# Kernel tuning notes

Measured on AMD Instinct MI355X. Metric: run time of the kernel, lower is better.

Reference implementation:

```python
import jax, jax.numpy as jnp
import numpy as np

N_HEADS = 16
EMB_DIM = 2048
HEAD_DIM = EMB_DIM // N_HEADS  # 128
SEQ_LEN = 2048


def _init_tensor(key, size, scale_dim=0):
    # matches torch: (2*rand - 1) / sqrt(size[scale_dim])
    u = jax.random.uniform(key, size, dtype=jnp.float32)
    return (2.0 * u - 1.0) / jnp.sqrt(jnp.float32(size[scale_dim]))


def setup_inputs() -> dict:
    key = jax.random.key(0)
    kx, kq, kk, kv, ko = jax.random.split(key, 5)
    X = jax.random.normal(kx, (1, SEQ_LEN, EMB_DIM), dtype=jnp.float32)
    W_Q = _init_tensor(kq, (N_HEADS, EMB_DIM, HEAD_DIM), scale_dim=1)
    W_K = _init_tensor(kk, (N_HEADS, EMB_DIM, HEAD_DIM), scale_dim=1)
    W_V = _init_tensor(kv, (N_HEADS, EMB_DIM, HEAD_DIM), scale_dim=1)
    W_out = _init_tensor(ko, (EMB_DIM, EMB_DIM), scale_dim=0)
    return {"X": X, "W_Q": W_Q, "W_K": W_K, "W_V": W_V, "W_out": W_out}


def reference(X, W_Q, W_K, W_V, W_out):
    # X: (1, t, d); W_Q/K/V: (n, d, h); broadcast matmul -> (n, t, h)
    x = X[0]  # (t, d)
    Q = jnp.einsum('td,ndh->nth', x, W_Q)
    K = jnp.einsum('td,ndh->nth', x, W_K)
    V = jnp.einsum('td,ndh->nth', x, W_V)
    scale = 1.0 / jnp.sqrt(jnp.float32(HEAD_DIM))
    Z = jnp.einsum('nth,nsh->nts', Q, K) * scale  # (n, t, t)
    A = jax.nn.softmax(Z, axis=-1)
    R = jnp.einsum('nts,nsh->nth', A, V)  # (n, t, h)
    t = R.shape[1]
    X_cat = jnp.transpose(R, (1, 0, 2)).reshape(t, N_HEADS * HEAD_DIM)  # (t, d)
    return X_cat @ W_out  # (t, d)
```

## Files before the change

### kernel.cpp

```cpp
#include <hip/hip_runtime.h>


typedef unsigned short u16;
typedef __bf16 bf16x8 __attribute__((ext_vector_type(8)));
typedef float f32x4 __attribute__((ext_vector_type(4)));
typedef __attribute__((address_space(1))) void gvoid;
typedef __attribute__((address_space(3))) void svoid;

union B8 { uint4 u; uint2 d[2]; bf16x8 b; };

__device__ __forceinline__ u16 f2b(float f) {
  unsigned int u = __float_as_uint(f);
  unsigned int r = (u + 0x7FFFu + ((u >> 16) & 1u)) >> 16;
  return (u16)r;
}

__global__ __launch_bounds__(256) void prep_kernel(const float* __restrict__ X,
                                                   const float* __restrict__ WQ,
                                                   const float* __restrict__ WK,
                                                   const float* __restrict__ WV,
                                                   const float* __restrict__ WO,
                                                   u16* __restrict__ Xb,
                                                   u16* __restrict__ Wqkvb,
                                                   u16* __restrict__ Woutb) {
  int bid = blockIdx.x;
  int seg = bid >> 12;
  int sub = bid & 4095;
  int tid = threadIdx.x;
  if (seg == 0) {
    int i = (sub * 256 + tid) * 4;
    float4 v = *(const float4*)(X + i);
    ushort4 o;
    o.x = f2b(v.x); o.y = f2b(v.y); o.z = f2b(v.z); o.w = f2b(v.w);
    *(ushort4*)(Xb + i) = o;
    return;
  }
  __shared__ float t[32][33];
  const float* S;
  u16* D;
  int N, n0, k0;
  if (seg <= 3) {
    const float* W = (seg == 1) ? WQ : (seg == 2) ? WK : WV;
    int head = sub >> 8, rest = sub & 255;
    N = 128;
    S = W + (size_t)head * 2048 * 128;
    D = Wqkvb + (size_t)(seg - 1) * 16 * 2048 * 128 + (size_t)head * 2048 * 128;
    n0 = (rest & 3) * 32;
    k0 = (rest >> 2) * 32;
  } else {
    N = 2048;
    S = WO;
    D = Woutb;
    n0 = (sub & 63) * 32;
    k0 = (sub >> 6) * 32;
  }
  int tx = tid & 31, ty = tid >> 5;
#pragma unroll
  for (int d = 0; d < 4; ++d)
    t[ty + d * 8][tx] = S[(size_t)(k0 + ty + d * 8) * N + n0 + tx];
  __syncthreads();
#pragma unroll
  for (int d = 0; d < 4; ++d)
    D[(size_t)(n0 + ty + d * 8) * 2048 + k0 + tx] = f2b(t[tx][ty + d * 8]);
}

__device__ __forceinline__ void stage_tile(const u16* Ag, const u16* Bg,
                                           u16* As, u16* Bs, int k0, int tid) {
#pragma unroll
  for (int it = 0; it < 4; ++it) {
    int s = it * 256 + tid;
    int pb = s * 16;
    int lb = pb ^ ((((pb) >> 7) & 7) << 4);
    int row = lb >> 7;
    int k8 = (lb >> 4) & 7;
    const u16* ga = Ag + (size_t)row * 2048 + k0 + k8 * 8;
    const u16* gb = Bg + (size_t)row * 2048 + k0 + k8 * 8;
    char* la = (char*)As + it * 4096 + (tid & 192) * 16;
    char* lb2 = (char*)Bs + it * 4096 + (tid & 192) * 16;
    __builtin_amdgcn_global_load_lds((gvoid*)(void*)ga, (svoid*)la, 16, 0, 0);
    __builtin_amdgcn_global_load_lds((gvoid*)(void*)gb, (svoid*)lb2, 16, 0, 0);
  }
}

__device__ __forceinline__ void compute_tile(const u16* As, const u16* Bs,
                                             f32x4 acc[4][4], int lane, int wr, int wc) {
#pragma unroll
  for (int ks = 0; ks < 2; ++ks) {
    B8 a[4], b[4];
#pragma unroll
    for (int i = 0; i < 4; ++i) {
      int rowa = wr * 64 + i * 16 + (lane & 15);
      int ba = rowa * 128 + ks * 64 + (lane >> 4) * 16;
      ba ^= (rowa & 7) << 4;
      a[i].u = *(const uint4*)((const char*)As + ba);
      int rowb = wc * 64 + i * 16 + (lane & 15);
      int bb = rowb * 128 + ks * 64 + (lane >> 4) * 16;
      bb ^= (rowb & 7) << 4;
      b[i].u = *(const uint4*)((const char*)Bs + bb);
    }
    __builtin_amdgcn_s_setprio(1);
#pragma unroll
    for (int i = 0; i < 4; ++i)
#pragma unroll
      for (int j = 0; j < 4; ++j)
        acc[i][j] = __builtin_amdgcn_mfma_f32_16x16x32_bf16(a[i].b, b[j].b, acc[i][j], 0, 0, 0);
    __builtin_amdgcn_s_setprio(0);
  }
}

__device__ __forceinline__ void gemm_mainloop(const u16* Ag, const u16* Bg,
                                              u16* As, u16* Bs,
                                              f32x4 acc[4][4], int tid) {
  const int lane = tid & 63;
  const int wr = tid >> 7, wc = (tid >> 6) & 1;
  for (int k0 = 0; k0 < 2048; k0 += 64) {
    __syncthreads();
    stage_tile(Ag, Bg, As, Bs, k0, tid);
    __syncthreads();
    compute_tile(As, Bs, acc, lane, wr, wc);
  }
}

__device__ __forceinline__ void gemm_mainloop_dbuf(const u16* Ag, const u16* Bg,
                                                   u16* As0, u16* Bs0, u16* As1, u16* Bs1,
                                                   f32x4 acc[4][4], int tid) {
  const int lane = tid & 63;
  const int wr = tid >> 7, wc = (tid >> 6) & 1;
  stage_tile(Ag, Bg, As0, Bs0, 0, tid);
  __syncthreads();
  for (int i = 0; i < 32; ++i) {
    u16* Ac = (i & 1) ? As1 : As0;
    u16* Bc = (i & 1) ? Bs1 : Bs0;
    u16* An = (i & 1) ? As0 : As1;
    u16* Bn = (i & 1) ? Bs0 : Bs1;
    if (i < 31) stage_tile(Ag, Bg, An, Bn, (i + 1) * 64, tid);
    compute_tile(Ac, Bc, acc, lane, wr, wc);
    __syncthreads();
  }
}

__global__ __launch_bounds__(256) void qkv_gemm_kernel(const u16* __restrict__ Xb,
                                                       const u16* __restrict__ Wb,
                                                       u16* __restrict__ Qb,
                                                       u16* __restrict__ Kb,
                                                       u16* __restrict__ VTb) {
  __shared__ __align__(16) u16 As[128 * 64];
  __shared__ __align__(16) u16 Bs[128 * 64];
  int tid = threadIdx.x;
  int o = blockIdx.x;
  int swz = (o & 7) * 96 + (o >> 3);
  int m0 = (swz & 15) * 128;
  int c0 = swz >> 4;
  int tau = c0 >> 4, head = c0 & 15;
  f32x4 z = {0.f, 0.f, 0.f, 0.f};
  f32x4 acc[4][4];
#pragma unroll
  for (int i = 0; i < 4; ++i)
#pragma unroll
    for (int j = 0; j < 4; ++j) acc[i][j] = z;
  gemm_mainloop(Xb + (size_t)m0 * 2048, Wb + (size_t)c0 * 128 * 2048, As, Bs, acc, tid);

  int lane = tid & 63, wr = tid >> 7, wc = (tid >> 6) & 1;
  if (tau < 2) {
    u16* Oh = ((tau == 0) ? Qb : Kb) + (size_t)head * 2048 * 128;
    float sc = (tau == 0) ? 0.08838834764831845f : 1.0f;
#pragma unroll
    for (int i = 0; i < 4; ++i) {
      int rb = m0 + wr * 64 + i * 16 + (lane >> 4) * 4;
#pragma unroll
      for (int j = 0; j < 4; ++j) {
        int col = wc * 64 + j * 16 + (lane & 15);
#pragma unroll
        for (int r = 0; r < 4; ++r)
          Oh[(size_t)(rb + r) * 128 + col] = f2b(acc[i][j][r] * sc);
      }
    }
  } else {
    u16* Vh = VTb + (size_t)head * 128 * 2048;
#pragma unroll
    for (int i = 0; i < 4; ++i) {
      int rb = m0 + wr * 64 + i * 16 + (lane >> 4) * 4;
#pragma unroll
      for (int j = 0; j < 4; ++j) {
        int col = wc * 64 + j * 16 + (lane & 15);
        ushort4 v;
        v.x = f2b(acc[i][j][0]); v.y = f2b(acc[i][j][1]);
        v.z = f2b(acc[i][j][2]); v.w = f2b(acc[i][j][3]);
        *(ushort4*)(Vh + (size_t)col * 2048 + rb) = v;
      }
    }
  }
}

__global__ __launch_bounds__(256, 2) void attn_kernel(const u16* __restrict__ Qb,
                                                      const u16* __restrict__ Kb,
                                                      const u16* __restrict__ VTb,
                                                      u16* __restrict__ Rb) {
  __shared__ __align__(16) u16 Ks[2][64 * 128];
  __shared__ __align__(16) u16 Vs[2][128 * 64];
  __shared__ __align__(16) u16 Ps[4 * 16 * 68];
  int tid = threadIdx.x, lane = tid & 63, w = tid >> 6;
  int bid = blockIdx.x;
  int swz = (bid & 7) * 64 + (bid >> 3);
  int head = swz >> 5;
  int q0 = (swz & 31) * 64;
  const u16* Qh = Qb + (size_t)head * 2048 * 128;
  const u16* Kh = Kb + (size_t)head * 2048 * 128;
  const u16* Vh = VTb + (size_t)head * 128 * 2048;

  B8 q[4];
  {
    int qrow = q0 + w * 16 + (lane & 15);
#pragma unroll
    for (int ks = 0; ks < 4; ++ks)
      q[ks].u = *(const uint4*)(Qh + (size_t)qrow * 128 + ks * 32 + (lane >> 4) * 8);
  }

  f32x4 o[8];
  f32x4 z4 = {0.f, 0.f, 0.f, 0.f};
#pragma unroll
  for (int f = 0; f < 8; ++f) o[f] = z4;
  float m_run[4] = {-1e30f, -1e30f, -1e30f, -1e30f};
  float l_run[4] = {0.f, 0.f, 0.f, 0.f};

  auto STAGE = [&](int bi, int s0) {
#pragma unroll
    for (int it2 = 0; it2 < 4; ++it2) {
      int pb = (it2 * 256 + tid) * 16;
      int lbK = pb ^ (((pb >> 8) & 7) << 4);
      int rowK = lbK >> 8;
      int k8 = (lbK >> 4) & 15;
      const u16* gk = Kh + (size_t)(s0 + rowK) * 128 + k8 * 8;
      char* dk = (char*)Ks[bi] + it2 * 4096 + (tid & 192) * 16;
      __builtin_amdgcn_global_load_lds((gvoid*)(void*)gk, (svoid*)dk, 16, 0, 0);
      int lbV = pb ^ (((pb >> 7) & 7) << 4);
      int rowV = lbV >> 7;
      int t8 = (lbV >> 4) & 7;
      const u16* gv = Vh + (size_t)rowV * 2048 + s0 + t8 * 8;
      char* dv = (char*)Vs[bi] + it2 * 4096 + (tid & 192) * 16;
      __builtin_amdgcn_global_load_lds((gvoid*)(void*)gv, (svoid*)dv, 16, 0, 0);
    }
  };

  STAGE(0, 0);
  __syncthreads();

  u16* Pw = Ps + w * 16 * 68;
  for (int it = 0; it < 32; ++it) {
    int cur = it & 1;
    if (it < 31) STAGE(cur ^ 1, (it + 1) * 64);

    f32x4 s[4];
#pragma unroll
    for (int f = 0; f < 4; ++f) s[f] = z4;
    __builtin_amdgcn_s_setprio(1);
#pragma unroll
    for (int f = 0; f < 4; ++f) {
      int r = f * 16 + (lane & 15);
#pragma unroll
      for (int ks = 0; ks < 4; ++ks) {
        int lb = r * 256 + ks * 64 + (lane >> 4) * 16;
        B8 kb;
        kb.u = *(const uint4*)((const char*)Ks[cur] + (lb ^ ((r & 7) << 4)));
        s[f] = __builtin_amdgcn_mfma_f32_16x16x32_bf16(q[ks].b, kb.b, s[f], 0, 0, 0);
      }
    }
    __builtin_amdgcn_s_setprio(0);

    float mt[4];
#pragma unroll
    for (int i = 0; i < 4; ++i)
      mt[i] = fmaxf(fmaxf(s[0][i], s[1][i]), fmaxf(s[2][i], s[3][i]));
#pragma unroll
    for (int mask = 1; mask <= 8; mask <<= 1)
#pragma unroll
      for (int i = 0; i < 4; ++i) mt[i] = fmaxf(mt[i], __shfl_xor(mt[i], mask, 64));

    float al[4];
#pragma unroll
    for (int i = 0; i < 4; ++i) {
      float mn = fmaxf(m_run[i], mt[i]);
      al[i] = __expf(m_run[i] - mn);
      m_run[i] = mn;
    }
    float ps[4] = {0.f, 0.f, 0.f, 0.f};
#pragma unroll
    for (int f = 0; f < 4; ++f)
#pragma unroll
      for (int i = 0; i < 4; ++i) {
        float p = __expf(s[f][i] - m_run[i]);
        ps[i] += p;
        Pw[((lane >> 4) * 4 + i) * 68 + f * 16 + (lane & 15)] = f2b(p);
      }
#pragma unroll
    for (int mask = 1; mask <= 8; mask <<= 1)
#pragma unroll
      for (int i = 0; i < 4; ++i) ps[i] += __shfl_xor(ps[i], mask, 64);
#pragma unroll
    for (int i = 0; i < 4; ++i) l_run[i] = l_run[i] * al[i] + ps[i];

#pragma unroll
    for (int f = 0; f < 8; ++f)
#pragma unroll
      for (int i = 0; i < 4; ++i) o[f][i] *= al[i];

    B8 pa[2];
#pragma unroll
    for (int k2 = 0; k2 < 2; ++k2) {
      const u16* pp = Pw + (lane & 15) * 68 + k2 * 32 + (lane >> 4) * 8;
      pa[k2].d[0] = *(const uint2*)(pp);
      pa[k2].d[1] = *(const uint2*)(pp + 4);
    }
    __builtin_amdgcn_s_setprio(1);
#pragma unroll
    for (int f = 0; f < 8; ++f) {
      int r = f * 16 + (lane & 15);
#pragma unroll
      for (int k2 = 0; k2 < 2; ++k2) {
        int lb = r * 128 + k2 * 64 + (lane >> 4) * 16;
        B8 vb;
        vb.u = *(const uint4*)((const char*)Vs[cur] + (lb ^ ((r & 7) << 4)));
        o[f] = __builtin_amdgcn_mfma_f32_16x16x32_bf16(pa[k2].b, vb.b, o[f], 0, 0, 0);
      }
    }
    __builtin_amdgcn_s_setprio(0);

    __syncthreads();
  }

#pragma unroll
  for (int i = 0; i < 4; ++i) {
    float inv = 1.0f / l_run[i];
    int row = q0 + w * 16 + (lane >> 4) * 4 + i;
#pragma unroll
    for (int f = 0; f < 8; ++f) {
      int col = head * 128 + f * 16 + (lane & 15);
      Rb[(size_t)row * 2048 + col] = f2b(o[f][i] * inv);
    }
  }
}

__global__ __launch_bounds__(256) void out_gemm_kernel(const u16* __restrict__ Rb,
                                                       const u16* __restrict__ Wob,
                                                       float* __restrict__ out) {
  __shared__ __align__(16) u16 As[2][128 * 64];
  __shared__ __align__(16) u16 Bs[2][128 * 64];
  int tid = threadIdx.x;
  int o = blockIdx.x;
  int swz = (o & 7) * 32 + (o >> 3);
  int m0 = (swz & 15) * 128, n0 = (swz >> 4) * 128;
  f32x4 z = {0.f, 0.f, 0.f, 0.f};
  f32x4 acc[4][4];
#pragma unroll
  for (int i = 0; i < 4; ++i)
#pragma unroll
    for (int j = 0; j < 4; ++j) acc[i][j] = z;
  gemm_mainloop_dbuf(Rb + (size_t)m0 * 2048, Wob + (size_t)n0 * 2048,
                     As[0], Bs[0], As[1], Bs[1], acc, tid);

  int lane = tid & 63, wr = tid >> 7, wc = (tid >> 6) & 1;
#pragma unroll
  for (int i = 0; i < 4; ++i) {
    int rb = m0 + wr * 64 + i * 16 + (lane >> 4) * 4;
#pragma unroll
    for (int j = 0; j < 4; ++j) {
      int col = n0 + wc * 64 + j * 16 + (lane & 15);
#pragma unroll
      for (int r = 0; r < 4; ++r)
        out[(size_t)(rb + r) * 2048 + col] = acc[i][j][r];
    }
  }
}

extern "C" void kernel_launch(void* const* d_in, const int* in_sizes, int n_in,
                              void* d_out, int out_size, void* d_ws, size_t ws_size,
                              hipStream_t stream) {
  const float* X  = (const float*)d_in[0];
  const float* WQ = (const float*)d_in[1];
  const float* WK = (const float*)d_in[2];
  const float* WV = (const float*)d_in[3];
  const float* WO = (const float*)d_in[4];
  float* out = (float*)d_out;

  char* ws = (char*)d_ws;
  const size_t MB8 = 8u << 20;
  u16* Xb    = (u16*)(ws);
  u16* Wqkvb = (u16*)(ws + MB8);
  u16* Woutb = (u16*)(ws + 4 * MB8);
  u16* Qb    = (u16*)(ws + 5 * MB8);
  u16* Kb    = (u16*)(ws + 6 * MB8);
  u16* VTb   = (u16*)(ws + 7 * MB8);
  u16* Rbuf  = (u16*)(ws + MB8);

  prep_kernel<<<dim3(20480), dim3(256), 0, stream>>>(X, WQ, WK, WV, WO, Xb, Wqkvb, Woutb);
  qkv_gemm_kernel<<<dim3(768), dim3(256), 0, stream>>>(Xb, Wqkvb, Qb, Kb, VTb);
  attn_kernel<<<dim3(512), dim3(256), 0, stream>>>(Qb, Kb, VTb, Rbuf);
  out_gemm_kernel<<<dim3(256), dim3(256), 0, stream>>>(Rbuf, Woutb, out);
}
```

Baseline: 315.9 us.

## Transpose attention MFMA layout to keep P in registers and skip rescaling

Swaps the MFMA operand order so each lane owns one query row, turning the row max and sum reductions into two cross-lane shuffles and leaving one running max and sum per lane. The P tile now goes from registers to the next MFMA through packed bf16 conversion and lane shuffles instead of an LDS round-trip. Output rescaling is skipped unless the max grows by more than a threshold, which cuts VALU work but lets unnormalized exponents grow before they are corrected. The final store becomes a vectorized ushort4 write per row.

```diff
diff --git a/kernel.cpp b/kernel.cpp
--- a/kernel.cpp
+++ b/kernel.cpp
@@ -7,7 +7,7 @@
 typedef __attribute__((address_space(1))) void gvoid;
 typedef __attribute__((address_space(3))) void svoid;
 
-union B8 { uint4 u; uint2 d[2]; bf16x8 b; };
+union B8 { uint4 u; uint2 d[2]; unsigned int w[4]; bf16x8 b; };
 
 __device__ __forceinline__ u16 f2b(float f) {
   unsigned int u = __float_as_uint(f);
@@ -198,7 +198,6 @@
                                                       u16* __restrict__ Rb) {
   __shared__ __align__(16) u16 Ks[2][64 * 128];
   __shared__ __align__(16) u16 Vs[2][128 * 64];
-  __shared__ __align__(16) u16 Ps[4 * 16 * 68];
   int tid = threadIdx.x, lane = tid & 63, w = tid >> 6;
   int bid = blockIdx.x;
   int swz = (bid & 7) * 64 + (bid >> 3);
@@ -207,6 +206,7 @@
   const u16* Qh = Qb + (size_t)head * 2048 * 128;
   const u16* Kh = Kb + (size_t)head * 2048 * 128;
   const u16* Vh = VTb + (size_t)head * 128 * 2048;
+  const int g = lane >> 4;
 
   B8 q[4];
   {
@@ -220,8 +220,7 @@
   f32x4 z4 = {0.f, 0.f, 0.f, 0.f};
 #pragma unroll
   for (int f = 0; f < 8; ++f) o[f] = z4;
-  float m_run[4] = {-1e30f, -1e30f, -1e30f, -1e30f};
-  float l_run[4] = {0.f, 0.f, 0.f, 0.f};
+  float m_run = -1e30f, l_run = 0.f;
 
   auto STAGE = [&](int bi, int s0) {
 #pragma unroll
@@ -245,7 +244,6 @@
   STAGE(0, 0);
   __syncthreads();
 
-  u16* Pw = Ps + w * 16 * 68;
   for (int it = 0; it < 32; ++it) {
     int cur = it & 1;
     if (it < 31) STAGE(cur ^ 1, (it + 1) * 64);
@@ -262,65 +260,82 @@
         int lb = r * 256 + ks * 64 + (lane >> 4) * 16;
         B8 kb;
         kb.u = *(const uint4*)((const char*)Ks[cur] + (lb ^ ((r & 7) << 4)));
-        s[f] = __builtin_amdgcn_mfma_f32_16x16x32_bf16(q[ks].b, kb.b, s[f], 0, 0, 0);
+        s[f] = __builtin_amdgcn_mfma_f32_16x16x32_bf16(kb.b, q[ks].b, s[f], 0, 0, 0);
       }
     }
     __builtin_amdgcn_s_setprio(0);
 
-    float mt[4];
-#pragma unroll
-    for (int i = 0; i < 4; ++i)
-      mt[i] = fmaxf(fmaxf(s[0][i], s[1][i]), fmaxf(s[2][i], s[3][i]));
-#pragma unroll
-    for (int mask = 1; mask <= 8; mask <<= 1)
-#pragma unroll
-      for (int i = 0; i < 4; ++i) mt[i] = fmaxf(mt[i], __shfl_xor(mt[i], mask, 64));
-
-    float al[4];
-#pragma unroll
-    for (int i = 0; i < 4; ++i) {
-      float mn = fmaxf(m_run[i], mt[i]);
-      al[i] = __expf(m_run[i] - mn);
-      m_run[i] = mn;
-    }
-    float ps[4] = {0.f, 0.f, 0.f, 0.f};
+    float mt = s[0][0];
 #pragma unroll
     for (int f = 0; f < 4; ++f)
 #pragma unroll
+      for (int i = 0; i < 4; ++i) mt = fmaxf(mt, s[f][i]);
+    mt = fmaxf(mt, __shfl_xor(mt, 16, 64));
+    mt = fmaxf(mt, __shfl_xor(mt, 32, 64));
+
+    if (!__all(mt - m_run <= 8.0f)) {
+      float mn = fmaxf(m_run, mt);
+      float al = __expf(m_run - mn);
+      m_run = mn;
+      l_run *= al;
+#pragma unroll
+      for (int f = 0; f < 8; ++f)
+#pragma unroll
+        for (int r = 0; r < 4; ++r) o[f][r] *= al;
+    }
+    float ps = 0.f;
+#pragma unroll
+    for (int f = 0; f < 4; ++f)
+#pragma unroll
       for (int i = 0; i < 4; ++i) {
-        float p = __expf(s[f][i] - m_run[i]);
-        ps[i] += p;
-        Pw[((lane >> 4) * 4 + i) * 68 + f * 16 + (lane & 15)] = f2b(p);
-      }
-#pragma unroll
-    for (int mask = 1; mask <= 8; mask <<= 1)
-#pragma unroll
-      for (int i = 0; i < 4; ++i) ps[i] += __shfl_xor(ps[i], mask, 64);
-#pragma unroll
-    for (int i = 0; i < 4; ++i) l_run[i] = l_run[i] * al[i] + ps[i];
-
-#pragma unroll
-    for (int f = 0; f < 8; ++f)
-#pragma unroll
-      for (int i = 0; i < 4; ++i) o[f][i] *= al[i];
-
-    B8 pa[2];
-#pragma unroll
-    for (int k2 = 0; k2 < 2; ++k2) {
-      const u16* pp = Pw + (lane & 15) * 68 + k2 * 32 + (lane >> 4) * 8;
-      pa[k2].d[0] = *(const uint2*)(pp);
-      pa[k2].d[1] = *(const uint2*)(pp + 4);
-    }
+        float p = __expf(s[f][i] - m_run);
+        ps += p;
+        s[f][i] = p;
+      }
+    ps += __shfl_xor(ps, 16, 64);
+    ps += __shfl_xor(ps, 32, 64);
+    l_run += ps;
+
+    unsigned int cl[4], ch[4];
+#pragma unroll
+    for (int f = 0; f < 4; ++f) {
+      asm("v_cvt_pk_bf16_f32 %0, %1, %2" : "=v"(cl[f]) : "v"(s[f][0]), "v"(s[f][1]));
+      asm("v_cvt_pk_bf16_f32 %0, %1, %2" : "=v"(ch[f]) : "v"(s[f][2]), "v"(s[f][3]));
+    }
+    int srcA = ((g & 1) << 5) | (lane & 15);
+    int srcB = srcA + 16;
+    int hi = g >> 1;
+    B8 pa0, pa1;
+    {
+      unsigned int a0 = __shfl((int)cl[0], srcA, 64), b0 = __shfl((int)cl[1], srcA, 64);
+      unsigned int a1 = __shfl((int)ch[0], srcA, 64), b1 = __shfl((int)ch[1], srcA, 64);
+      unsigned int a2 = __shfl((int)cl[0], srcB, 64), b2 = __shfl((int)cl[1], srcB, 64);
+      unsigned int a3 = __shfl((int)ch[0], srcB, 64), b3 = __shfl((int)ch[1], srcB, 64);
+      pa0.w[0] = hi ? b0 : a0; pa0.w[1] = hi ? b1 : a1;
+      pa0.w[2] = hi ? b2 : a2; pa0.w[3] = hi ? b3 : a3;
+      unsigned int c0 = __shfl((int)cl[2], srcA, 64), d0 = __shfl((int)cl[3], srcA, 64);
+      unsigned int c1 = __shfl((int)ch[2], srcA, 64), d1 = __shfl((int)ch[3], srcA, 64);
+      unsigned int c2 = __shfl((int)cl[2], srcB, 64), d2 = __shfl((int)cl[3], srcB, 64);
+      unsigned int c3 = __shfl((int)ch[2], srcB, 64), d3 = __shfl((int)ch[3], srcB, 64);
+      pa1.w[0] = hi ? d0 : c0; pa1.w[1] = hi ? d1 : c1;
+      pa1.w[2] = hi ? d2 : c2; pa1.w[3] = hi ? d3 : c3;
+    }
+
     __builtin_amdgcn_s_setprio(1);
 #pragma unroll
     for (int f = 0; f < 8; ++f) {
       int r = f * 16 + (lane & 15);
-#pragma unroll
-      for (int k2 = 0; k2 < 2; ++k2) {
-        int lb = r * 128 + k2 * 64 + (lane >> 4) * 16;
+      {
+        int lb = r * 128 + 0 * 64 + (lane >> 4) * 16;
         B8 vb;
         vb.u = *(const uint4*)((const char*)Vs[cur] + (lb ^ ((r & 7) << 4)));
-        o[f] = __builtin_amdgcn_mfma_f32_16x16x32_bf16(pa[k2].b, vb.b, o[f], 0, 0, 0);
+        o[f] = __builtin_amdgcn_mfma_f32_16x16x32_bf16(vb.b, pa0.b, o[f], 0, 0, 0);
+      }
+      {
+        int lb = r * 128 + 1 * 64 + (lane >> 4) * 16;
+        B8 vb;
+        vb.u = *(const uint4*)((const char*)Vs[cur] + (lb ^ ((r & 7) << 4)));
+        o[f] = __builtin_amdgcn_mfma_f32_16x16x32_bf16(vb.b, pa1.b, o[f], 0, 0, 0);
       }
     }
     __builtin_amdgcn_s_setprio(0);
@@ -328,15 +343,14 @@
     __syncthreads();
   }
 
-#pragma unroll
-  for (int i = 0; i < 4; ++i) {
-    float inv = 1.0f / l_run[i];
-    int row = q0 + w * 16 + (lane >> 4) * 4 + i;
-#pragma unroll
-    for (int f = 0; f < 8; ++f) {
-      int col = head * 128 + f * 16 + (lane & 15);
-      Rb[(size_t)row * 2048 + col] = f2b(o[f][i] * inv);
-    }
+  float inv = 1.0f / l_run;
+  int row = q0 + w * 16 + (lane & 15);
+#pragma unroll
+  for (int f = 0; f < 8; ++f) {
+    ushort4 v;
+    v.x = f2b(o[f][0] * inv); v.y = f2b(o[f][1] * inv);
+    v.z = f2b(o[f][2] * inv); v.w = f2b(o[f][3] * inv);
+    *(ushort4*)(Rb + (size_t)row * 2048 + head * 128 + f * 16 + g * 4) = v;
   }
 }
 
```

Result: faster. 300.3 us (-5.0%).
